# Kernel tuning notes

Hardware: AMD Instinct MI355X
Metric: run time of the kernel (lower is better)

Reference implementation:

```python
import jax, jax.numpy as jnp
import numpy as np
from jax import lax

DN = ('NCDHW', 'OIDHW', 'NCDHW')


def conv3(x, w, stride=1):
    return lax.conv_general_dilated(x, w, (stride,) * 3, 'VALID', dimension_numbers=DN)


def edge_pad(v):  # zero-gradient (Neumann) halo of width 1
    return jnp.pad(v, ((0, 0), (0, 0), (1, 1), (1, 1), (1, 1)), mode='edge')


def zero_pad(v):  # Dirichlet-0 halo for the MG correction
    return jnp.pad(v, ((0, 0), (0, 0), (1, 1), (1, 1), (1, 1)))


def bc_u(u, ub):  # Neumann everywhere, Dirichlet inlet (u=ub) on -x face
    p = edge_pad(u)
    return p.at[:, :, :, :, 0].set(jnp.asarray(ub, p.dtype))


def prol(x):  # nearest-neighbour upsample x2 (nn.Upsample scale_factor=2)
    for ax in (2, 3, 4):
        x = jnp.repeat(x, 2, axis=ax)
    return x


def setup_inputs() -> dict:
    N = 128
    key = jax.random.key(0)
    k = jax.random.split(key, 6)
    shp = (1, 1, N, N, N)
    # 7-point Laplacian stencil (A and diff)
    wA = np.zeros((1, 1, 3, 3, 3), np.float32)
    wA[0, 0, 1, 1, 1] = -6.0
    for d, h, w in [(0, 1, 1), (2, 1, 1), (1, 0, 1), (1, 2, 1), (1, 1, 0), (1, 1, 2)]:
        wA[0, 0, d, h, w] = 1.0
    w_diff = wA.copy()
    # central-difference advection stencils along W (x), H (y), D (z)
    w_xadv = np.zeros((1, 1, 3, 3, 3), np.float32)
    w_xadv[0, 0, 1, 1, 0], w_xadv[0, 0, 1, 1, 2] = -0.5, 0.5
    w_yadv = np.zeros((1, 1, 3, 3, 3), np.float32)
    w_yadv[0, 0, 1, 0, 1], w_yadv[0, 0, 1, 2, 1] = -0.5, 0.5
    w_zadv = np.zeros((1, 1, 3, 3, 3), np.float32)
    w_zadv[0, 0, 0, 1, 1], w_zadv[0, 0, 2, 1, 1] = -0.5, 0.5
    w_res = np.full((1, 1, 2, 2, 2), 0.125, np.float32)
    return {
        'values_u': jax.random.normal(k[0], shp, jnp.float32) * 0.1,
        'values_v': jax.random.normal(k[1], shp, jnp.float32) * 0.1,
        'values_w': jax.random.normal(k[2], shp, jnp.float32) * 0.1,
        'values_p': jax.random.normal(k[3], shp, jnp.float32) * 0.1,
        'sigma': jax.random.uniform(k[4], shp, jnp.float32) * 10.0,  # solid-body drag field
        'dt': jnp.asarray(0.05, jnp.float32),
        'wA': jnp.asarray(wA), 'w_diff': jnp.asarray(w_diff),
        'w_xadv': jnp.asarray(w_xadv), 'w_yadv': jnp.asarray(w_yadv),
        'w_zadv': jnp.asarray(w_zadv), 'w_res': jnp.asarray(w_res),
        'ub': 1, 'Re': 1, 'iteration': 2, 'nlevel': 9,
    }


def reference(values_u, values_v, values_w, values_p, sigma, dt,
              wA, w_diff, w_xadv, w_yadv, w_zadv, w_res,
              ub, Re, iteration, nlevel):
    diag = wA[0, 0, 1, 1, 1]
    A = lambda x: conv3(x, wA)
    diff = lambda x: conv3(x, w_diff)
    xadv = lambda x: conv3(x, w_xadv)
    yadv = lambda x: conv3(x, w_yadv)
    zadv = lambda x: conv3(x, w_zadv)
    res = lambda x: conv3(x, w_res, stride=2)

    def solid(u, v, w):
        f = 1.0 / (1.0 + dt * sigma)
        return u * f, v * f, w * f

    def pg(uu, vv, ww, u, v, w):  # Petrov-Galerkin dissipation (k fields == 1)
        one = jnp.ones_like(u)
        kp = edge_pad(one)
        ku = 0.5 * (one * diff(uu) + diff(uu * kp) - u * diff(kp))
        kv = 0.5 * (one * diff(vv) + diff(vv * kp) - v * diff(kp))
        kw = 0.5 * (one * diff(ww) + diff(ww * kp) - w * diff(kp))
        return ku, kv, kw

    u, v, w = solid(values_u, values_v, values_w)
    uu, vv, ww = bc_u(u, ub), edge_pad(v), edge_pad(w)
    pp = edge_pad(values_p)
    ku, kv, kw = pg(uu, vv, ww, u, v, w)
    # half-step predictor
    b_u = u + 0.5 * (Re * ku * dt - u * xadv(uu) * dt - v * yadv(uu) * dt - w * zadv(uu) * dt) - xadv(pp) * dt
    b_v = v + 0.5 * (Re * kv * dt - u * xadv(vv) * dt - v * yadv(vv) * dt - w * zadv(vv) * dt) - yadv(pp) * dt
    b_w = w + 0.5 * (Re * kw * dt - u * xadv(ww) * dt - v * yadv(ww) * dt - w * zadv(ww) * dt) - zadv(pp) * dt
    b_u, b_v, b_w = solid(b_u, b_v, b_w)
    buu, bvv, bww = bc_u(b_u, ub), edge_pad(b_v), edge_pad(b_w)
    ku, kv, kw = pg(buu, bvv, bww, b_u, b_v, b_w)
    # full-step corrector
    u = u + Re * ku * dt - b_u * xadv(buu) * dt - b_v * yadv(buu) * dt - b_w * zadv(buu) * dt - xadv(pp) * dt
    v = v + Re * kv * dt - b_u * xadv(bvv) * dt - b_v * yadv(bvv) * dt - b_w * zadv(bvv) * dt - yadv(pp) * dt
    w = w + Re * kw * dt - b_u * xadv(bww) * dt - b_v * yadv(bww) * dt - b_w * zadv(bww) * dt - zadv(pp) * dt
    u, v, w = solid(u, v, w)
    uu, vv, ww = bc_u(u, ub), edge_pad(v), edge_pad(w)
    # multigrid F-cycle pressure solve
    b = -(xadv(uu) + yadv(vv) + zadv(ww)) / dt
    p = values_p
    wmg = jnp.zeros((1, 1, 1, 1, 1), u.dtype)
    r = b
    for _ in range(iteration):
        wmg = jnp.zeros((1, 1, 1, 1, 1), u.dtype)
        r = A(pp) - b
        r_s = [r]
        for _i in range(1, nlevel - 1):
            r = res(r)
            r_s.append(r)
        for i in reversed(range(1, nlevel - 1)):
            wp = zero_pad(wmg)
            wmg = wmg - A(wp) / diag + r_s[i] / diag
            wmg = prol(wmg)
        p = p - wmg
        p = p - A(pp) / diag + b / diag
        pp = edge_pad(p)
    u = u - xadv(pp) * dt
    v = v - yadv(pp) * dt
    w = w - zadv(pp) * dt
    u, v, w = solid(u, v, w)
    return u, v, w, p, wmg, r
```

## Files before the change

kernel.cpp:

```cpp
#include <hip/hip_runtime.h>

#define NN 128
#define VV (NN*NN*NN)

typedef float v4 __attribute__((ext_vector_type(4)));
typedef unsigned short u16;

__device__ __forceinline__ float rcpf(float a){ return __builtin_amdgcn_rcpf(a); }
__device__ __forceinline__ v4 rcp4(v4 a){ v4 r; r.x=rcpf(a.x); r.y=rcpf(a.y); r.z=rcpf(a.z); r.w=rcpf(a.w); return r; }
__device__ __forceinline__ v4 mk4(float a,float b,float c,float d){ v4 r; r.x=a;r.y=b;r.z=c;r.w=d; return r; }
__device__ __forceinline__ int clampi(int a, int lo, int hi){ return min(max(a,lo),hi); }

__device__ __forceinline__ float b2f(u16 h){ union{unsigned u; float f;} c; c.u=((unsigned)h)<<16; return c.f; }
__device__ __forceinline__ u16 f2b(float f){
    union{float f; unsigned u;} c; c.f=f;
    unsigned rb = ((c.u>>16)&1u) + 0x7FFFu;
    return (u16)((c.u + rb)>>16);
}
__device__ __forceinline__ float ld1(const float* __restrict__ p, int o){ return p[o]; }
__device__ __forceinline__ float ld1(const u16*  __restrict__ p, int o){ return b2f(p[o]); }
__device__ __forceinline__ v4 ld4(const float* __restrict__ p, int o){ return *(const v4*)(p+o); }
__device__ __forceinline__ v4 ld4(const u16*  __restrict__ p, int o){
    ushort4 h = *(const ushort4*)(p+o);
    return mk4(b2f(h.x),b2f(h.y),b2f(h.z),b2f(h.w));
}
__device__ __forceinline__ void st4(float* __restrict__ p, int o, v4 v){ *(v4*)(p+o) = v; }
__device__ __forceinline__ void st4(u16*  __restrict__ p, int o, v4 v){
    ushort4 h; h.x=f2b(v.x); h.y=f2b(v.y); h.z=f2b(v.z); h.w=f2b(v.w);
    *(ushort4*)(p+o) = h;
}
template<typename T>
__device__ __forceinline__ float ldcT(const T* __restrict__ f, int z, int y, int x){
    z=clampi(z,0,NN-1); y=clampi(y,0,NN-1); x=clampi(x,0,NN-1);
    return ld1(f,(z*NN+y)*NN+x);
}

#define SETUP_OFFS \
    int i4 = (blockIdx.x*blockDim.x + threadIdx.x)<<2; \
    int x = i4 & 127, y = (i4>>7)&127, z = i4>>14; \
    bool x0 = (x==0), x1 = (x==124); \
    int o_c  = i4; \
    int o_ym = o_c + ((y>0)   ? -128   : 0); \
    int o_yp = o_c + ((y<127) ?  128   : 0); \
    int o_zm = o_c + ((z>0)   ? -16384 : 0); \
    int o_zp = o_c + ((z<127) ?  16384 : 0); \
    int o_xm = x0 ? o_c : o_c-1; \
    int o_xp = x1 ? o_c : o_c+4;

__global__ void __launch_bounds__(256) k_predict(
        const float* __restrict__ u_in, const float* __restrict__ v_in,
        const float* __restrict__ w_in, const float* __restrict__ p,
        const float* __restrict__ sg, const float* __restrict__ dtp,
        const int* __restrict__ ubp, const int* __restrict__ rep,
        u16* __restrict__ bu, u16* __restrict__ bv, u16* __restrict__ bw){
    SETUP_OFFS
    float dt = dtp[0], ub = (float)ubp[0], Re = (float)rep[0];
    float h = 0.5f*dt;

    v4 f_c  = rcp4(1.0f + dt*ld4(sg,o_c));
    v4 f_ym = rcp4(1.0f + dt*ld4(sg,o_ym));
    v4 f_yp = rcp4(1.0f + dt*ld4(sg,o_yp));
    v4 f_zm = rcp4(1.0f + dt*ld4(sg,o_zm));
    v4 f_zp = rcp4(1.0f + dt*ld4(sg,o_zp));
    float f_xm = rcpf(1.0f + dt*sg[o_xm]);
    float f_xp = rcpf(1.0f + dt*sg[o_xp]);

#define STEN(F, cen, vxm, vxp, vym, vyp, vzm, vzp, XMVAL) \
    v4 cen = ld4(F,o_c)*f_c; \
    v4 vym = ld4(F,o_ym)*f_ym; v4 vyp = ld4(F,o_yp)*f_yp; \
    v4 vzm = ld4(F,o_zm)*f_zm; v4 vzp = ld4(F,o_zp)*f_zp; \
    float cen##_xms = x0 ? (XMVAL) : F[o_xm]*f_xm; \
    float cen##_xps = x1 ? cen.w   : F[o_xp]*f_xp; \
    v4 vxm = mk4(cen##_xms, cen.x, cen.y, cen.z); \
    v4 vxp = mk4(cen.y, cen.z, cen.w, cen##_xps);

    STEN(u_in, uc, uxm, uxp, uym, uyp, uzm, uzp, ub)
    STEN(v_in, vc, vxm, vxp, vym, vyp, vzm, vzp, vc.x)
    STEN(w_in, wc, wxm, wxp, wym, wyp, wzm, wzp, wc.x)
#undef STEN

    v4 pc = ld4(p,o_c);
    v4 pym = ld4(p,o_ym), pyp = ld4(p,o_yp), pzm = ld4(p,o_zm), pzp = ld4(p,o_zp);
    float p_xms = x0 ? pc.x : p[o_xm];
    float p_xps = x1 ? pc.w : p[o_xp];
    v4 pxm = mk4(p_xms, pc.x, pc.y, pc.z);
    v4 pxp = mk4(pc.y, pc.z, pc.w, p_xps);
    v4 gpx = 0.5f*(pxp-pxm), gpy = 0.5f*(pyp-pym), gpz = 0.5f*(pzp-pzm);

    v4 lap_u = uxm+uxp+uym+uyp+uzm+uzp - 6.0f*uc;
    v4 lap_v = vxm+vxp+vym+vyp+vzm+vzp - 6.0f*vc;
    v4 lap_w = wxm+wxp+wym+wyp+wzm+wzp - 6.0f*wc;
    v4 xau=0.5f*(uxp-uxm), yau=0.5f*(uyp-uym), zau=0.5f*(uzp-uzm);
    v4 xav=0.5f*(vxp-vxm), yav=0.5f*(vyp-vym), zav=0.5f*(vzp-vzm);
    v4 xaw=0.5f*(wxp-wxm), yaw=0.5f*(wyp-wym), zaw=0.5f*(wzp-wzm);

    st4(bu,o_c, (uc + h*(Re*lap_u - (uc*xau + vc*yau + wc*zau)) - dt*gpx)*f_c);
    st4(bv,o_c, (vc + h*(Re*lap_v - (uc*xav + vc*yav + wc*zav)) - dt*gpy)*f_c);
    st4(bw,o_c, (wc + h*(Re*lap_w - (uc*xaw + vc*yaw + wc*zaw)) - dt*gpz)*f_c);
}

__global__ void __launch_bounds__(256) k_corr(
        const float* __restrict__ u_in, const float* __restrict__ v_in,
        const float* __restrict__ w_in,
        const u16* __restrict__ bu, const u16* __restrict__ bv,
        const u16* __restrict__ bw, const float* __restrict__ p,
        const float* __restrict__ sg, const float* __restrict__ dtp,
        const int* __restrict__ ubp, const int* __restrict__ rep,
        u16* __restrict__ ou, u16* __restrict__ ov, u16* __restrict__ ow){
    SETUP_OFFS
    float dt = dtp[0], ub = (float)ubp[0], Re = (float)rep[0];
    v4 f0 = rcp4(1.0f + dt*ld4(sg,o_c));
    v4 u0c = ld4(u_in,o_c)*f0, v0c = ld4(v_in,o_c)*f0, w0c = ld4(w_in,o_c)*f0;

#define STEN2(F, cen, vxm, vxp, vym, vyp, vzm, vzp, XMVAL) \
    v4 cen = ld4(F,o_c); \
    v4 vym = ld4(F,o_ym), vyp = ld4(F,o_yp), vzm = ld4(F,o_zm), vzp = ld4(F,o_zp); \
    float cen##_xms = x0 ? (XMVAL) : ld1(F,o_xm); \
    float cen##_xps = x1 ? cen.w   : ld1(F,o_xp); \
    v4 vxm = mk4(cen##_xms, cen.x, cen.y, cen.z); \
    v4 vxp = mk4(cen.y, cen.z, cen.w, cen##_xps);

    STEN2(bu, uc, uxm, uxp, uym, uyp, uzm, uzp, ub)
    STEN2(bv, vc, vxm, vxp, vym, vyp, vzm, vzp, vc.x)
    STEN2(bw, wc, wxm, wxp, wym, wyp, wzm, wzp, wc.x)
#undef STEN2

    v4 pc = ld4(p,o_c);
    v4 pym = ld4(p,o_ym), pyp = ld4(p,o_yp), pzm = ld4(p,o_zm), pzp = ld4(p,o_zp);
    float p_xms = x0 ? pc.x : p[o_xm];
    float p_xps = x1 ? pc.w : p[o_xp];
    v4 pxm = mk4(p_xms, pc.x, pc.y, pc.z);
    v4 pxp = mk4(pc.y, pc.z, pc.w, p_xps);
    v4 gpx = 0.5f*(pxp-pxm), gpy = 0.5f*(pyp-pym), gpz = 0.5f*(pzp-pzm);

    v4 lap_u = uxm+uxp+uym+uyp+uzm+uzp - 6.0f*uc;
    v4 lap_v = vxm+vxp+vym+vyp+vzm+vzp - 6.0f*vc;
    v4 lap_w = wxm+wxp+wym+wyp+wzm+wzp - 6.0f*wc;
    v4 xau=0.5f*(uxp-uxm), yau=0.5f*(uyp-uym), zau=0.5f*(uzp-uzm);
    v4 xav=0.5f*(vxp-vxm), yav=0.5f*(vyp-vym), zav=0.5f*(vzp-vzm);
    v4 xaw=0.5f*(wxp-wxm), yaw=0.5f*(wyp-wym), zaw=0.5f*(wzp-wzm);

    st4(ou,o_c, (u0c + dt*(Re*lap_u - (uc*xau + vc*yau + wc*zau)) - dt*gpx)*f0);
    st4(ov,o_c, (v0c + dt*(Re*lap_v - (uc*xav + vc*yav + wc*zav)) - dt*gpy)*f0);
    st4(ow,o_c, (w0c + dt*(Re*lap_w - (uc*xaw + vc*yaw + wc*zaw)) - dt*gpz)*f0);
}

__global__ void __launch_bounds__(256) k_div(
        const u16* __restrict__ u, const u16* __restrict__ v,
        const u16* __restrict__ w, const float* __restrict__ dtp,
        const int* __restrict__ ubp, u16* __restrict__ b){
    SETUP_OFFS
    float dt = dtp[0], ub = (float)ubp[0];
    v4 ucv = ld4(u,o_c);
    float u_xms = x0 ? ub    : ld1(u,o_xm);
    float u_xps = x1 ? ucv.w : ld1(u,o_xp);
    v4 uxm = mk4(u_xms, ucv.x, ucv.y, ucv.z);
    v4 uxp = mk4(ucv.y, ucv.z, ucv.w, u_xps);
    v4 vym = ld4(v,o_ym), vyp = ld4(v,o_yp);
    v4 wzm = ld4(w,o_zm), wzp = ld4(w,o_zp);
    v4 div = 0.5f*((uxp-uxm)+(vyp-vym)+(wzp-wzm));
    st4(b,o_c, -div*rcpf(dt));
}

template<typename PT>
__global__ void k_rr(const PT* __restrict__ p, const u16* __restrict__ b, float* __restrict__ r1){
    int i = blockIdx.x*blockDim.x + threadIdx.x;
    if (i >= 64*64*64) return;
    int X = i & 63, Y = (i>>6)&63, Z = i>>12;
    float acc = 0.f;
    #pragma unroll
    for (int dz=0;dz<2;++dz)
      #pragma unroll
      for (int dy=0;dy<2;++dy)
        #pragma unroll
        for (int dx=0;dx<2;++dx){
            int z=2*Z+dz, y=2*Y+dy, x=2*X+dx;
            float pc = ld1(p,(z*128+y)*128+x);
            float lap = ldcT(p,z,y,x-1)+ldcT(p,z,y,x+1)+ldcT(p,z,y-1,x)+ldcT(p,z,y+1,x)
                      + ldcT(p,z-1,y,x)+ldcT(p,z+1,y,x) - 6.0f*pc;
            acc += lap - ld1(b,(z*128+y)*128+x);
        }
    r1[i] = 0.125f*acc;
}

__global__ void k_r2(const float* __restrict__ r1, float* __restrict__ r2){
    int c = blockIdx.x*blockDim.x + threadIdx.x;
    if (c >= 32*32*32) return;
    int X = c & 31, Y = (c>>5)&31, Z = c>>10;
    float a = 0.f;
    #pragma unroll
    for (int dz=0;dz<2;++dz)
      #pragma unroll
      for (int dy=0;dy<2;++dy)
        #pragma unroll
        for (int dx=0;dx<2;++dx)
            a += r1[((2*Z+dz)*64 + (2*Y+dy))*64 + (2*X+dx)];
    r2[c] = 0.125f*a;
}

__device__ void chain_restrict(const float* __restrict__ src, float* __restrict__ dst,
                               int nd, int t, int nt){
    int nd3 = nd*nd*nd, ns = nd*2;
    for (int c = t; c < nd3; c += nt){
        int X = c % nd, Y = (c/nd) % nd, Z = c/(nd*nd);
        float a = 0.f;
        for (int dz=0;dz<2;++dz)
          for (int dy=0;dy<2;++dy)
            for (int dx=0;dx<2;++dx)
                a += src[((2*Z+dz)*ns + (2*Y+dy))*ns + (2*X+dx)];
        dst[c] = 0.125f*a;
    }
}
__device__ void chain_jacobi(const float* __restrict__ jin, const float* __restrict__ r,
                             float* __restrict__ jout, int n, int t, int nt){
    int n3 = n*n*n, hn = n>>1;
    for (int c = t; c < n3; c += nt){
        int X = c % n, Y = (c/n) % n, Z = c/(n*n);
        float s = 0.f;
        s += (X>0  ) ? jin[((Z>>1)*hn+(Y>>1))*hn+((X-1)>>1)] : 0.f;
        s += (X<n-1) ? jin[((Z>>1)*hn+(Y>>1))*hn+((X+1)>>1)] : 0.f;
        s += (Y>0  ) ? jin[((Z>>1)*hn+((Y-1)>>1))*hn+(X>>1)] : 0.f;
        s += (Y<n-1) ? jin[((Z>>1)*hn+((Y+1)>>1))*hn+(X>>1)] : 0.f;
        s += (Z>0  ) ? jin[(((Z-1)>>1)*hn+(Y>>1))*hn+(X>>1)] : 0.f;
        s += (Z<n-1) ? jin[(((Z+1)>>1)*hn+(Y>>1))*hn+(X>>1)] : 0.f;
        jout[c] = (s - r[c]) * (1.0f/6.0f);
    }
}

__global__ void __launch_bounds__(1024) k_chain(const float* __restrict__ r2,
                                                float* __restrict__ j3g, float* __restrict__ r7g){
    __shared__ float r3[4096], r4[512], r5[64], r6[8];
    __shared__ float j7[1], j6[8], j5[64], j4[512], j3[4096];
    int t = threadIdx.x; const int nt = 1024;
    chain_restrict(r2, r3, 16, t, nt); __syncthreads();
    chain_restrict(r3, r4,  8, t, nt); __syncthreads();
    chain_restrict(r4, r5,  4, t, nt); __syncthreads();
    chain_restrict(r5, r6,  2, t, nt); __syncthreads();
    if (t == 0){
        float a = 0.f;
        for (int k=0;k<8;++k) a += r6[k];
        float r7 = 0.125f*a;
        r7g[0] = r7;
        j7[0] = -r7*(1.0f/6.0f);
    }
    __syncthreads();
    chain_jacobi(j7, r6, j6,  2, t, nt); __syncthreads();
    chain_jacobi(j6, r5, j5,  4, t, nt); __syncthreads();
    chain_jacobi(j5, r4, j4,  8, t, nt); __syncthreads();
    chain_jacobi(j4, r3, j3, 16, t, nt); __syncthreads();
    for (int c = t; c < 4096; c += nt) j3g[c] = j3[c];
}

__global__ void k_j2(const float* __restrict__ j3, const float* __restrict__ r2,
                     float* __restrict__ j2){
    int c = blockIdx.x*blockDim.x + threadIdx.x;
    if (c >= 32*32*32) return;
    int X = c & 31, Y = (c>>5)&31, Z = c>>10;
    float s = 0.f;
    s += (X>0 ) ? j3[((Z>>1)*16+(Y>>1))*16+((X-1)>>1)] : 0.f;
    s += (X<31) ? j3[((Z>>1)*16+(Y>>1))*16+((X+1)>>1)] : 0.f;
    s += (Y>0 ) ? j3[((Z>>1)*16+((Y-1)>>1))*16+(X>>1)] : 0.f;
    s += (Y<31) ? j3[((Z>>1)*16+((Y+1)>>1))*16+(X>>1)] : 0.f;
    s += (Z>0 ) ? j3[(((Z-1)>>1)*16+(Y>>1))*16+(X>>1)] : 0.f;
    s += (Z<31) ? j3[(((Z+1)>>1)*16+(Y>>1))*16+(X>>1)] : 0.f;
    j2[c] = (s - r2[c]) * (1.0f/6.0f);
}

__device__ __forceinline__ float j1_eval(const float* __restrict__ r1, const float* __restrict__ j2,
                                         int X, int Y, int Z){
    float s = 0.f;
    s += (X>0 ) ? j2[((Z>>1)*32+(Y>>1))*32+((X-1)>>1)] : 0.f;
    s += (X<63) ? j2[((Z>>1)*32+(Y>>1))*32+((X+1)>>1)] : 0.f;
    s += (Y>0 ) ? j2[((Z>>1)*32+((Y-1)>>1))*32+(X>>1)] : 0.f;
    s += (Y<63) ? j2[((Z>>1)*32+((Y+1)>>1))*32+(X>>1)] : 0.f;
    s += (Z>0 ) ? j2[(((Z-1)>>1)*32+(Y>>1))*32+(X>>1)] : 0.f;
    s += (Z<63) ? j2[(((Z+1)>>1)*32+(Y>>1))*32+(X>>1)] : 0.f;
    return (s - r1[(Z*64+Y)*64+X]) * (1.0f/6.0f);
}

template<typename PT>
__global__ void __launch_bounds__(256) k_pupd(
        const PT* __restrict__ p, const float* __restrict__ r1,
        const float* __restrict__ j2, const u16* __restrict__ b,
        u16* __restrict__ pout){
    SETUP_OFFS
    v4 pc = ld4(p,o_c);
    v4 pym = ld4(p,o_ym), pyp = ld4(p,o_yp), pzm = ld4(p,o_zm), pzp = ld4(p,o_zp);
    float p_xms = x0 ? pc.x : ld1(p,o_xm);
    float p_xps = x1 ? pc.w : ld1(p,o_xp);
    v4 pxm = mk4(p_xms, pc.x, pc.y, pc.z);
    v4 pxp = mk4(pc.y, pc.z, pc.w, p_xps);
    v4 lap = pxm+pxp+pym+pyp+pzm+pzp - 6.0f*pc;
    v4 b4 = ld4(b,o_c);
    float j1a = j1_eval(r1, j2, (x>>1),   y>>1, z>>1);
    float j1b = j1_eval(r1, j2, (x>>1)+1, y>>1, z>>1);
    v4 j1v = mk4(j1a, j1a, j1b, j1b);
    st4(pout,o_c, pc - j1v + (lap - b4)*(1.0f/6.0f));
}

__global__ void __launch_bounds__(256) k_final(
        const u16* __restrict__ u, const u16* __restrict__ v,
        const u16* __restrict__ w, const u16* __restrict__ p,
        const float* __restrict__ r1, const float* __restrict__ j2,
        const float* __restrict__ r7, const float* __restrict__ sg,
        const float* __restrict__ dtp, float* __restrict__ out){
    SETUP_OFFS
    float dt = dtp[0];
    v4 pc = ld4(p,o_c);
    v4 pym = ld4(p,o_ym), pyp = ld4(p,o_yp), pzm = ld4(p,o_zm), pzp = ld4(p,o_zp);
    float p_xms = x0 ? pc.x : ld1(p,o_xm);
    float p_xps = x1 ? pc.w : ld1(p,o_xp);
    v4 pxm = mk4(p_xms, pc.x, pc.y, pc.z);
    v4 pxp = mk4(pc.y, pc.z, pc.w, p_xps);
    v4 gpx = 0.5f*(pxp-pxm), gpy = 0.5f*(pyp-pym), gpz = 0.5f*(pzp-pzm);
    v4 f0 = rcp4(1.0f + dt*ld4(sg,o_c));
    st4(out, o_c,                        (ld4(u,o_c) - dt*gpx)*f0);
    st4(out + (size_t)VV, o_c,           (ld4(v,o_c) - dt*gpy)*f0);
    st4(out + 2*(size_t)VV, o_c,         (ld4(w,o_c) - dt*gpz)*f0);
    st4(out + 3*(size_t)VV, o_c,         pc);
    float j1a = j1_eval(r1, j2, (x>>1),   y>>1, z>>1);
    float j1b = j1_eval(r1, j2, (x>>1)+1, y>>1, z>>1);
    st4(out + 4*(size_t)VV, o_c,         mk4(j1a, j1a, j1b, j1b));
    if (i4 == 0) out[5*(size_t)VV] = r7[0];
}

extern "C" void kernel_launch(void* const* d_in, const int* in_sizes, int n_in,
                              void* d_out, int out_size, void* d_ws, size_t ws_size,
                              hipStream_t stream){
    (void)in_sizes; (void)n_in; (void)out_size; (void)ws_size;
    const float* u_in = (const float*)d_in[0];
    const float* v_in = (const float*)d_in[1];
    const float* w_in = (const float*)d_in[2];
    const float* p_in = (const float*)d_in[3];
    const float* sg   = (const float*)d_in[4];
    const float* dtp  = (const float*)d_in[5];
    const int*  ubp   = (const int*)d_in[12];
    const int*  rep   = (const int*)d_in[13];

    u16* wh = (u16*)d_ws;
    const size_t V = VV;
    u16* bu = wh;
    u16* bv = wh +   V;
    u16* bw = wh + 2*V;
    u16* u  = wh + 3*V;
    u16* v  = wh + 4*V;
    u16* w  = wh + 5*V;
    u16* b  = wh + 6*V;
    u16* P1 = wh + 7*V;
    u16* P2 = wh + 8*V;
    float* fs = (float*)(wh + 10*V);
    float* r1 = fs;
    float* r2 = r1 + 64*64*64;
    float* j2 = r2 + 32*32*32;
    float* j3 = j2 + 32*32*32;
    float* r7 = j3 + 16*16*16;

    dim3 blk(256);
    int g4 = (VV/4)/256;

    k_predict<<<g4, blk, 0, stream>>>(u_in,v_in,w_in,p_in,sg,dtp,ubp,rep,bu,bv,bw);
    k_corr   <<<g4, blk, 0, stream>>>(u_in,v_in,w_in,bu,bv,bw,p_in,sg,dtp,ubp,rep,u,v,w);
    k_div    <<<g4, blk, 0, stream>>>(u,v,w,dtp,ubp,b);

    k_rr<float><<<(64*64*64)/256, blk, 0, stream>>>(p_in, b, r1);
    k_r2        <<<(32*32*32)/256, blk, 0, stream>>>(r1, r2);
    k_chain     <<<1, 1024, 0, stream>>>(r2, j3, r7);
    k_j2        <<<(32*32*32)/256, blk, 0, stream>>>(j3, r2, j2);
    k_pupd<float><<<g4, blk, 0, stream>>>(p_in, r1, j2, b, P1);

    k_rr<u16>  <<<(64*64*64)/256, blk, 0, stream>>>(P1, b, r1);
    k_r2       <<<(32*32*32)/256, blk, 0, stream>>>(r1, r2);
    k_chain    <<<1, 1024, 0, stream>>>(r2, j3, r7);
    k_j2       <<<(32*32*32)/256, blk, 0, stream>>>(j3, r2, j2);
    k_pupd<u16><<<g4, blk, 0, stream>>>(P1, r1, j2, b, P2);

    k_final<<<g4, blk, 0, stream>>>(u,v,w,P2,r1,j2,r7,sg,dtp,(float*)d_out);
}
```

Before: 205.4 us.

## Fuse multigrid stages into tiled kernels with last-block coarse chain

Replaces the chain of divergence, restriction, coarse-chain, prolongation and pressure-update kernels with three tiled kernels on 16^3 blocks. The restrictions run through shared memory, and the last block to finish (found with an atomic counter) runs the coarse-grid chain. The pressure update is recomputed on a halo-padded shared tile and fed straight into the next residual or the final projection, so the P2 buffer and many launches disappear. The costs are redundant halo recomputation, a serial coarse chain inside one block that adds to the tail, and heavy shared-memory use at 512 threads per block, which limits occupancy.

```diff
diff --git a/kernel.cpp b/kernel.cpp
--- a/kernel.cpp
+++ b/kernel.cpp
@@ -2,6 +2,7 @@
 
 #define NN 128
 #define VV (NN*NN*NN)
+#define GRID_MG 512
 
 typedef float v4 __attribute__((ext_vector_type(4)));
 typedef unsigned short u16;
@@ -52,8 +53,10 @@
         const float* __restrict__ w_in, const float* __restrict__ p,
         const float* __restrict__ sg, const float* __restrict__ dtp,
         const int* __restrict__ ubp, const int* __restrict__ rep,
-        u16* __restrict__ bu, u16* __restrict__ bv, u16* __restrict__ bw){
+        u16* __restrict__ bu, u16* __restrict__ bv, u16* __restrict__ bw,
+        int* __restrict__ cnt){
     SETUP_OFFS
+    if (i4 == 0){ cnt[0] = 0; cnt[1] = 0; }
     float dt = dtp[0], ub = (float)ubp[0], Re = (float)rep[0];
     float h = 0.5f*dt;
 
@@ -145,57 +148,16 @@
     st4(ow,o_c, (w0c + dt*(Re*lap_w - (uc*xaw + vc*yaw + wc*zaw)) - dt*gpz)*f0);
 }
 
-__global__ void __launch_bounds__(256) k_div(
-        const u16* __restrict__ u, const u16* __restrict__ v,
-        const u16* __restrict__ w, const float* __restrict__ dtp,
-        const int* __restrict__ ubp, u16* __restrict__ b){
-    SETUP_OFFS
-    float dt = dtp[0], ub = (float)ubp[0];
-    v4 ucv = ld4(u,o_c);
-    float u_xms = x0 ? ub    : ld1(u,o_xm);
-    float u_xps = x1 ? ucv.w : ld1(u,o_xp);
-    v4 uxm = mk4(u_xms, ucv.x, ucv.y, ucv.z);
-    v4 uxp = mk4(ucv.y, ucv.z, ucv.w, u_xps);
-    v4 vym = ld4(v,o_ym), vyp = ld4(v,o_yp);
-    v4 wzm = ld4(w,o_zm), wzp = ld4(w,o_zp);
-    v4 div = 0.5f*((uxp-uxm)+(vyp-vym)+(wzp-wzm));
-    st4(b,o_c, -div*rcpf(dt));
-}
-
-template<typename PT>
-__global__ void k_rr(const PT* __restrict__ p, const u16* __restrict__ b, float* __restrict__ r1){
-    int i = blockIdx.x*blockDim.x + threadIdx.x;
-    if (i >= 64*64*64) return;
-    int X = i & 63, Y = (i>>6)&63, Z = i>>12;
-    float acc = 0.f;
-    #pragma unroll
-    for (int dz=0;dz<2;++dz)
-      #pragma unroll
-      for (int dy=0;dy<2;++dy)
-        #pragma unroll
-        for (int dx=0;dx<2;++dx){
-            int z=2*Z+dz, y=2*Y+dy, x=2*X+dx;
-            float pc = ld1(p,(z*128+y)*128+x);
-            float lap = ldcT(p,z,y,x-1)+ldcT(p,z,y,x+1)+ldcT(p,z,y-1,x)+ldcT(p,z,y+1,x)
-                      + ldcT(p,z-1,y,x)+ldcT(p,z+1,y,x) - 6.0f*pc;
-            acc += lap - ld1(b,(z*128+y)*128+x);
-        }
-    r1[i] = 0.125f*acc;
-}
-
-__global__ void k_r2(const float* __restrict__ r1, float* __restrict__ r2){
-    int c = blockIdx.x*blockDim.x + threadIdx.x;
-    if (c >= 32*32*32) return;
-    int X = c & 31, Y = (c>>5)&31, Z = c>>10;
-    float a = 0.f;
-    #pragma unroll
-    for (int dz=0;dz<2;++dz)
-      #pragma unroll
-      for (int dy=0;dy<2;++dy)
-        #pragma unroll
-        for (int dx=0;dx<2;++dx)
-            a += r1[((2*Z+dz)*64 + (2*Y+dy))*64 + (2*X+dx)];
-    r2[c] = 0.125f*a;
+__device__ __forceinline__ float j1_eval(const float* __restrict__ r1, const float* __restrict__ j2,
+                                         int X, int Y, int Z){
+    float s = 0.f;
+    s += (X>0 ) ? j2[((Z>>1)*32+(Y>>1))*32+((X-1)>>1)] : 0.f;
+    s += (X<63) ? j2[((Z>>1)*32+(Y>>1))*32+((X+1)>>1)] : 0.f;
+    s += (Y>0 ) ? j2[((Z>>1)*32+((Y-1)>>1))*32+(X>>1)] : 0.f;
+    s += (Y<63) ? j2[((Z>>1)*32+((Y+1)>>1))*32+(X>>1)] : 0.f;
+    s += (Z>0 ) ? j2[(((Z-1)>>1)*32+(Y>>1))*32+(X>>1)] : 0.f;
+    s += (Z<63) ? j2[(((Z+1)>>1)*32+(Y>>1))*32+(X>>1)] : 0.f;
+    return (s - r1[(Z*64+Y)*64+X]) * (1.0f/6.0f);
 }
 
 __device__ void chain_restrict(const float* __restrict__ src, float* __restrict__ dst,
@@ -227,101 +189,252 @@
     }
 }
 
-__global__ void __launch_bounds__(1024) k_chain(const float* __restrict__ r2,
-                                                float* __restrict__ j3g, float* __restrict__ r7g){
-    __shared__ float r3[4096], r4[512], r5[64], r6[8];
-    __shared__ float j7[1], j6[8], j5[64], j4[512], j3[4096];
-    int t = threadIdx.x; const int nt = 1024;
-    chain_restrict(r2, r3, 16, t, nt); __syncthreads();
-    chain_restrict(r3, r4,  8, t, nt); __syncthreads();
-    chain_restrict(r4, r5,  4, t, nt); __syncthreads();
-    chain_restrict(r5, r6,  2, t, nt); __syncthreads();
+struct ChainSmem {
+    float r3[4096], r4[512], r5[64], r6[8];
+    float j7[1], j6[8], j5[64], j4[512], j3[4096];
+};
+
+__device__ void run_chain(ChainSmem& S, const float* __restrict__ r2g,
+                          float* __restrict__ j2, float* __restrict__ r7,
+                          int t, int nt){
+    chain_restrict(r2g, S.r3, 16, t, nt); __syncthreads();
+    chain_restrict(S.r3, S.r4,  8, t, nt); __syncthreads();
+    chain_restrict(S.r4, S.r5,  4, t, nt); __syncthreads();
+    chain_restrict(S.r5, S.r6,  2, t, nt); __syncthreads();
     if (t == 0){
         float a = 0.f;
-        for (int k=0;k<8;++k) a += r6[k];
-        float r7 = 0.125f*a;
-        r7g[0] = r7;
-        j7[0] = -r7*(1.0f/6.0f);
-    }
-    __syncthreads();
-    chain_jacobi(j7, r6, j6,  2, t, nt); __syncthreads();
-    chain_jacobi(j6, r5, j5,  4, t, nt); __syncthreads();
-    chain_jacobi(j5, r4, j4,  8, t, nt); __syncthreads();
-    chain_jacobi(j4, r3, j3, 16, t, nt); __syncthreads();
-    for (int c = t; c < 4096; c += nt) j3g[c] = j3[c];
-}
-
-__global__ void k_j2(const float* __restrict__ j3, const float* __restrict__ r2,
-                     float* __restrict__ j2){
-    int c = blockIdx.x*blockDim.x + threadIdx.x;
-    if (c >= 32*32*32) return;
-    int X = c & 31, Y = (c>>5)&31, Z = c>>10;
-    float s = 0.f;
-    s += (X>0 ) ? j3[((Z>>1)*16+(Y>>1))*16+((X-1)>>1)] : 0.f;
-    s += (X<31) ? j3[((Z>>1)*16+(Y>>1))*16+((X+1)>>1)] : 0.f;
-    s += (Y>0 ) ? j3[((Z>>1)*16+((Y-1)>>1))*16+(X>>1)] : 0.f;
-    s += (Y<31) ? j3[((Z>>1)*16+((Y+1)>>1))*16+(X>>1)] : 0.f;
-    s += (Z>0 ) ? j3[(((Z-1)>>1)*16+(Y>>1))*16+(X>>1)] : 0.f;
-    s += (Z<31) ? j3[(((Z+1)>>1)*16+(Y>>1))*16+(X>>1)] : 0.f;
-    j2[c] = (s - r2[c]) * (1.0f/6.0f);
-}
-
-__device__ __forceinline__ float j1_eval(const float* __restrict__ r1, const float* __restrict__ j2,
-                                         int X, int Y, int Z){
-    float s = 0.f;
-    s += (X>0 ) ? j2[((Z>>1)*32+(Y>>1))*32+((X-1)>>1)] : 0.f;
-    s += (X<63) ? j2[((Z>>1)*32+(Y>>1))*32+((X+1)>>1)] : 0.f;
-    s += (Y>0 ) ? j2[((Z>>1)*32+((Y-1)>>1))*32+(X>>1)] : 0.f;
-    s += (Y<63) ? j2[((Z>>1)*32+((Y+1)>>1))*32+(X>>1)] : 0.f;
-    s += (Z>0 ) ? j2[(((Z-1)>>1)*32+(Y>>1))*32+(X>>1)] : 0.f;
-    s += (Z<63) ? j2[(((Z+1)>>1)*32+(Y>>1))*32+(X>>1)] : 0.f;
-    return (s - r1[(Z*64+Y)*64+X]) * (1.0f/6.0f);
+        for (int k=0;k<8;++k) a += S.r6[k];
+        float rv = 0.125f*a;
+        r7[0] = rv;
+        S.j7[0] = -rv*(1.0f/6.0f);
+    }
+    __syncthreads();
+    chain_jacobi(S.j7, S.r6, S.j6,  2, t, nt); __syncthreads();
+    chain_jacobi(S.j6, S.r5, S.j5,  4, t, nt); __syncthreads();
+    chain_jacobi(S.j5, S.r4, S.j4,  8, t, nt); __syncthreads();
+    chain_jacobi(S.j4, S.r3, S.j3, 16, t, nt); __syncthreads();
+    for (int c = t; c < 32*32*32; c += nt){
+        int X = c & 31, Y = (c>>5)&31, Z = c>>10;
+        const float* j3 = S.j3;
+        float s = 0.f;
+        s += (X>0 ) ? j3[((Z>>1)*16+(Y>>1))*16+((X-1)>>1)] : 0.f;
+        s += (X<31) ? j3[((Z>>1)*16+(Y>>1))*16+((X+1)>>1)] : 0.f;
+        s += (Y>0 ) ? j3[((Z>>1)*16+((Y-1)>>1))*16+(X>>1)] : 0.f;
+        s += (Y<31) ? j3[((Z>>1)*16+((Y+1)>>1))*16+(X>>1)] : 0.f;
+        s += (Z>0 ) ? j3[(((Z-1)>>1)*16+(Y>>1))*16+(X>>1)] : 0.f;
+        s += (Z<31) ? j3[(((Z+1)>>1)*16+(Y>>1))*16+(X>>1)] : 0.f;
+        j2[c] = (s - r2g[c]) * (1.0f/6.0f);
+    }
 }
 
 template<typename PT>
-__global__ void __launch_bounds__(256) k_pupd(
-        const PT* __restrict__ p, const float* __restrict__ r1,
-        const float* __restrict__ j2, const u16* __restrict__ b,
-        u16* __restrict__ pout){
-    SETUP_OFFS
-    v4 pc = ld4(p,o_c);
-    v4 pym = ld4(p,o_ym), pyp = ld4(p,o_yp), pzm = ld4(p,o_zm), pzp = ld4(p,o_zp);
-    float p_xms = x0 ? pc.x : ld1(p,o_xm);
-    float p_xps = x1 ? pc.w : ld1(p,o_xp);
-    v4 pxm = mk4(p_xms, pc.x, pc.y, pc.z);
-    v4 pxp = mk4(pc.y, pc.z, pc.w, p_xps);
-    v4 lap = pxm+pxp+pym+pyp+pzm+pzp - 6.0f*pc;
-    v4 b4 = ld4(b,o_c);
-    float j1a = j1_eval(r1, j2, (x>>1),   y>>1, z>>1);
-    float j1b = j1_eval(r1, j2, (x>>1)+1, y>>1, z>>1);
-    v4 j1v = mk4(j1a, j1a, j1b, j1b);
-    st4(pout,o_c, pc - j1v + (lap - b4)*(1.0f/6.0f));
-}
-
-__global__ void __launch_bounds__(256) k_final(
-        const u16* __restrict__ u, const u16* __restrict__ v,
-        const u16* __restrict__ w, const u16* __restrict__ p,
-        const float* __restrict__ r1, const float* __restrict__ j2,
+__device__ void build_P(float* __restrict__ Ps, const PT* __restrict__ p,
+                        const u16* __restrict__ b,
+                        const float* __restrict__ r1x, const float* __restrict__ j2x,
+                        int bx0, int by0, int bz0, int t,
+                        u16* __restrict__ P1out, float* __restrict__ pout){
+    for (int idx = t; idx < 18*18*18; idx += 512){
+        int lx = idx % 18; int tmp = idx/18; int ly = tmp % 18; int lz = tmp/18;
+        int gx = clampi(bx0+lx,0,NN-1), gy = clampi(by0+ly,0,NN-1), gz = clampi(bz0+lz,0,NN-1);
+        int gi = (gz*NN+gy)*NN+gx;
+        float pc = ld1(p, gi);
+        float lap = ldcT(p,gz,gy,gx-1)+ldcT(p,gz,gy,gx+1)+ldcT(p,gz,gy-1,gx)+ldcT(p,gz,gy+1,gx)
+                  + ldcT(p,gz-1,gy,gx)+ldcT(p,gz+1,gy,gx) - 6.0f*pc;
+        float bb = ld1(b, gi);
+        float jv = j1_eval(r1x, j2x, gx>>1, gy>>1, gz>>1);
+        float val = pc - jv + (lap - bb)*(1.0f/6.0f);
+        Ps[idx] = val;
+        if (lx>0 && lx<17 && ly>0 && ly<17 && lz>0 && lz<17){
+            if (P1out) P1out[gi] = f2b(val);
+            if (pout)  pout[gi]  = val;
+        }
+    }
+}
+
+__global__ void __launch_bounds__(512) k_mg1(
+        const u16* __restrict__ u, const u16* __restrict__ v, const u16* __restrict__ w,
+        const float* __restrict__ p, const float* __restrict__ dtp,
+        const int* __restrict__ ubp,
+        u16* __restrict__ b, float* __restrict__ r1, float* __restrict__ r2g,
+        float* __restrict__ j2, float* __restrict__ r7, int* __restrict__ cnt){
+    __shared__ float b_s[16*16*16];
+    __shared__ float r1_s[8*8*8];
+    __shared__ ChainSmem CS;
+    __shared__ int s_last;
+    int t = threadIdx.x;
+    int BX = blockIdx.x & 7, BY = (blockIdx.x>>3)&7, BZ = blockIdx.x>>6;
+    float dt = dtp[0], ub = (float)ubp[0];
+    float rdt = rcpf(dt);
+
+    {
+        int tx4 = t & 3, fy = (t>>2)&15, fz0 = t>>6;
+        int gx = BX*16 + tx4*4, gy = BY*16 + fy;
+        for (int k=0;k<2;++k){
+            int fz = fz0 + 8*k, gz = BZ*16 + fz;
+            int o_c = (gz*NN+gy)*NN + gx;
+            bool x0 = (gx==0), x1 = (gx==124);
+            int o_ym = o_c + ((gy>0)    ? -NN    : 0);
+            int o_yp = o_c + ((gy<NN-1) ?  NN    : 0);
+            int o_zm = o_c + ((gz>0)    ? -NN*NN : 0);
+            int o_zp = o_c + ((gz<NN-1) ?  NN*NN : 0);
+            int o_xm = x0 ? o_c : o_c-1, o_xp = x1 ? o_c : o_c+4;
+            v4 ucv = ld4(u,o_c);
+            float u_xms = x0 ? ub    : ld1(u,o_xm);
+            float u_xps = x1 ? ucv.w : ld1(u,o_xp);
+            v4 uxm = mk4(u_xms, ucv.x, ucv.y, ucv.z);
+            v4 uxp = mk4(ucv.y, ucv.z, ucv.w, u_xps);
+            v4 vym = ld4(v,o_ym), vyp = ld4(v,o_yp);
+            v4 wzm = ld4(w,o_zm), wzp = ld4(w,o_zp);
+            v4 db = -(0.5f*((uxp-uxm)+(vyp-vym)+(wzp-wzm)))*rdt;
+            st4(b,o_c,db);
+            *(v4*)&b_s[(fz*16+fy)*16 + tx4*4] = db;
+        }
+    }
+    __syncthreads();
+    {
+        int CX = t&7, CY = (t>>3)&7, CZ = t>>6;
+        int GX = BX*8+CX, GY = BY*8+CY, GZ = BZ*8+CZ;
+        float acc = 0.f;
+        #pragma unroll
+        for (int dz=0;dz<2;++dz)
+        #pragma unroll
+        for (int dy=0;dy<2;++dy)
+        #pragma unroll
+        for (int dx=0;dx<2;++dx){
+            int z = 2*GZ+dz, y = 2*GY+dy, x = 2*GX+dx;
+            float pc = p[(z*NN+y)*NN+x];
+            float lap = ldcT(p,z,y,x-1)+ldcT(p,z,y,x+1)+ldcT(p,z,y-1,x)+ldcT(p,z,y+1,x)
+                      + ldcT(p,z-1,y,x)+ldcT(p,z+1,y,x) - 6.0f*pc;
+            acc += lap - b_s[((2*CZ+dz)*16+(2*CY+dy))*16+(2*CX+dx)];
+        }
+        float rv = 0.125f*acc;
+        r1[(GZ*64+GY)*64+GX] = rv;
+        r1_s[(CZ*8+CY)*8+CX] = rv;
+    }
+    __syncthreads();
+    if (t < 64){
+        int X = t&3, Y = (t>>2)&3, Z = t>>4;
+        float a = 0.f;
+        #pragma unroll
+        for (int dz=0;dz<2;++dz)
+        #pragma unroll
+        for (int dy=0;dy<2;++dy)
+        #pragma unroll
+        for (int dx=0;dx<2;++dx)
+            a += r1_s[((2*Z+dz)*8+(2*Y+dy))*8+(2*X+dx)];
+        r2g[((BZ*4+Z)*32 + (BY*4+Y))*32 + (BX*4+X)] = 0.125f*a;
+    }
+    __threadfence();
+    __syncthreads();
+    if (t == 0) s_last = (atomicAdd(cnt,1) == GRID_MG-1) ? 1 : 0;
+    __syncthreads();
+    if (!s_last) return;
+    __threadfence();
+    run_chain(CS, r2g, j2, r7, t, 512);
+}
+
+__global__ void __launch_bounds__(512) k_mg2(
+        const float* __restrict__ p, const u16* __restrict__ b,
+        const float* __restrict__ r1a, float* __restrict__ j2,
+        u16* __restrict__ P1, float* __restrict__ r1b,
+        float* __restrict__ r2g, float* __restrict__ r7, int* __restrict__ cnt){
+    __shared__ float Ps[18*18*18];
+    __shared__ float r1_s[8*8*8];
+    __shared__ ChainSmem CS;
+    __shared__ int s_last;
+    int t = threadIdx.x;
+    int BX = blockIdx.x & 7, BY = (blockIdx.x>>3)&7, BZ = blockIdx.x>>6;
+    int bx0 = BX*16-1, by0 = BY*16-1, bz0 = BZ*16-1;
+
+    build_P<float>(Ps, p, b, r1a, j2, bx0,by0,bz0, t, P1, (float*)0);
+    __syncthreads();
+    {
+        int CX = t&7, CY = (t>>3)&7, CZ = t>>6;
+        int GX = BX*8+CX, GY = BY*8+CY, GZ = BZ*8+CZ;
+        float acc = 0.f;
+        #pragma unroll
+        for (int dz=0;dz<2;++dz)
+        #pragma unroll
+        for (int dy=0;dy<2;++dy)
+        #pragma unroll
+        for (int dx=0;dx<2;++dx){
+            int x = 2*GX+dx, y = 2*GY+dy, z = 2*GZ+dz;
+            int lx = x-bx0, ly = y-by0, lz = z-bz0;
+            int lxm = clampi(x-1,0,NN-1)-bx0, lxp = clampi(x+1,0,NN-1)-bx0;
+            int lym = clampi(y-1,0,NN-1)-by0, lyp = clampi(y+1,0,NN-1)-by0;
+            int lzm = clampi(z-1,0,NN-1)-bz0, lzp = clampi(z+1,0,NN-1)-bz0;
+            float pc = Ps[(lz*18+ly)*18+lx];
+            float lap = Ps[(lz*18+ly)*18+lxm] + Ps[(lz*18+ly)*18+lxp]
+                      + Ps[(lz*18+lym)*18+lx] + Ps[(lz*18+lyp)*18+lx]
+                      + Ps[(lzm*18+ly)*18+lx] + Ps[(lzp*18+ly)*18+lx] - 6.0f*pc;
+            acc += lap - ld1(b,(z*NN+y)*NN+x);
+        }
+        float rv = 0.125f*acc;
+        r1b[(GZ*64+GY)*64+GX] = rv;
+        r1_s[(CZ*8+CY)*8+CX] = rv;
+    }
+    __syncthreads();
+    if (t < 64){
+        int X = t&3, Y = (t>>2)&3, Z = t>>4;
+        float a = 0.f;
+        #pragma unroll
+        for (int dz=0;dz<2;++dz)
+        #pragma unroll
+        for (int dy=0;dy<2;++dy)
+        #pragma unroll
+        for (int dx=0;dx<2;++dx)
+            a += r1_s[((2*Z+dz)*8+(2*Y+dy))*8+(2*X+dx)];
+        r2g[((BZ*4+Z)*32 + (BY*4+Y))*32 + (BX*4+X)] = 0.125f*a;
+    }
+    __threadfence();
+    __syncthreads();
+    if (t == 0) s_last = (atomicAdd(cnt,1) == GRID_MG-1) ? 1 : 0;
+    __syncthreads();
+    if (!s_last) return;
+    __threadfence();
+    run_chain(CS, r2g, j2, r7, t, 512);
+}
+
+__global__ void __launch_bounds__(512) k_fin(
+        const u16* __restrict__ u, const u16* __restrict__ v, const u16* __restrict__ w,
+        const u16* __restrict__ P1, const u16* __restrict__ b,
+        const float* __restrict__ r1b, const float* __restrict__ j2,
         const float* __restrict__ r7, const float* __restrict__ sg,
         const float* __restrict__ dtp, float* __restrict__ out){
-    SETUP_OFFS
+    __shared__ float Ps[18*18*18];
+    int t = threadIdx.x;
+    int BX = blockIdx.x & 7, BY = (blockIdx.x>>3)&7, BZ = blockIdx.x>>6;
+    int bx0 = BX*16-1, by0 = BY*16-1, bz0 = BZ*16-1;
+
+    build_P<u16>(Ps, P1, b, r1b, j2, bx0,by0,bz0, t, (u16*)0, out + 3*(size_t)VV);
+    __syncthreads();
+
     float dt = dtp[0];
-    v4 pc = ld4(p,o_c);
-    v4 pym = ld4(p,o_ym), pyp = ld4(p,o_yp), pzm = ld4(p,o_zm), pzp = ld4(p,o_zp);
-    float p_xms = x0 ? pc.x : ld1(p,o_xm);
-    float p_xps = x1 ? pc.w : ld1(p,o_xp);
-    v4 pxm = mk4(p_xms, pc.x, pc.y, pc.z);
-    v4 pxp = mk4(pc.y, pc.z, pc.w, p_xps);
-    v4 gpx = 0.5f*(pxp-pxm), gpy = 0.5f*(pyp-pym), gpz = 0.5f*(pzp-pzm);
-    v4 f0 = rcp4(1.0f + dt*ld4(sg,o_c));
-    st4(out, o_c,                        (ld4(u,o_c) - dt*gpx)*f0);
-    st4(out + (size_t)VV, o_c,           (ld4(v,o_c) - dt*gpy)*f0);
-    st4(out + 2*(size_t)VV, o_c,         (ld4(w,o_c) - dt*gpz)*f0);
-    st4(out + 3*(size_t)VV, o_c,         pc);
-    float j1a = j1_eval(r1, j2, (x>>1),   y>>1, z>>1);
-    float j1b = j1_eval(r1, j2, (x>>1)+1, y>>1, z>>1);
-    st4(out + 4*(size_t)VV, o_c,         mk4(j1a, j1a, j1b, j1b));
-    if (i4 == 0) out[5*(size_t)VV] = r7[0];
+    int tx4 = t & 3, fy = (t>>2)&15, fz0 = t>>6;
+    for (int k=0;k<2;++k){
+        int fz = fz0 + 8*k;
+        int gx = BX*16 + tx4*4, gy = BY*16 + fy, gz = BZ*16 + fz;
+        int o_c = (gz*NN+gy)*NN + gx;
+        int lx = tx4*4+1, ly = fy+1, lz = fz+1;
+        int rb  = (lz*18+ly)*18;
+        float pA = Ps[rb+lx-1], pB = Ps[rb+lx],   pC = Ps[rb+lx+1];
+        float pD = Ps[rb+lx+2], pE = Ps[rb+lx+3], pF = Ps[rb+lx+4];
+        v4 gpx = 0.5f*mk4(pC-pA, pD-pB, pE-pC, pF-pD);
+        int rym = (lz*18+(ly-1))*18, ryp = (lz*18+(ly+1))*18;
+        v4 gpy = 0.5f*mk4(Ps[ryp+lx  ]-Ps[rym+lx  ], Ps[ryp+lx+1]-Ps[rym+lx+1],
+                          Ps[ryp+lx+2]-Ps[rym+lx+2], Ps[ryp+lx+3]-Ps[rym+lx+3]);
+        int rzm = ((lz-1)*18+ly)*18, rzp = ((lz+1)*18+ly)*18;
+        v4 gpz = 0.5f*mk4(Ps[rzp+lx  ]-Ps[rzm+lx  ], Ps[rzp+lx+1]-Ps[rzm+lx+1],
+                          Ps[rzp+lx+2]-Ps[rzm+lx+2], Ps[rzp+lx+3]-Ps[rzm+lx+3]);
+        v4 f0 = rcp4(1.0f + dt*ld4(sg,o_c));
+        st4(out,                o_c, (ld4(u,o_c) - dt*gpx)*f0);
+        st4(out +   (size_t)VV, o_c, (ld4(v,o_c) - dt*gpy)*f0);
+        st4(out + 2*(size_t)VV, o_c, (ld4(w,o_c) - dt*gpz)*f0);
+        float j1a = j1_eval(r1b, j2, (gx>>1),   gy>>1, gz>>1);
+        float j1c = j1_eval(r1b, j2, (gx>>1)+1, gy>>1, gz>>1);
+        st4(out + 4*(size_t)VV, o_c, mk4(j1a, j1a, j1c, j1c));
+    }
+    if (blockIdx.x == 0 && t == 0) out[5*(size_t)VV] = r7[0];
 }
 
 extern "C" void kernel_launch(void* const* d_in, const int* in_sizes, int n_in,
@@ -347,32 +460,20 @@
     u16* w  = wh + 5*V;
     u16* b  = wh + 6*V;
     u16* P1 = wh + 7*V;
-    u16* P2 = wh + 8*V;
-    float* fs = (float*)(wh + 10*V);
-    float* r1 = fs;
-    float* r2 = r1 + 64*64*64;
-    float* j2 = r2 + 32*32*32;
-    float* j3 = j2 + 32*32*32;
-    float* r7 = j3 + 16*16*16;
+    float* fs  = (float*)(wh + 8*V);
+    float* r1a = fs;
+    float* r1b = r1a + 64*64*64;
+    float* r2  = r1b + 64*64*64;
+    float* j2  = r2  + 32*32*32;
+    float* r7  = j2  + 32*32*32;
+    int*   cnt = (int*)(r7 + 1);
 
     dim3 blk(256);
     int g4 = (VV/4)/256;
 
-    k_predict<<<g4, blk, 0, stream>>>(u_in,v_in,w_in,p_in,sg,dtp,ubp,rep,bu,bv,bw);
+    k_predict<<<g4, blk, 0, stream>>>(u_in,v_in,w_in,p_in,sg,dtp,ubp,rep,bu,bv,bw,cnt);
     k_corr   <<<g4, blk, 0, stream>>>(u_in,v_in,w_in,bu,bv,bw,p_in,sg,dtp,ubp,rep,u,v,w);
-    k_div    <<<g4, blk, 0, stream>>>(u,v,w,dtp,ubp,b);
-
-    k_rr<float><<<(64*64*64)/256, blk, 0, stream>>>(p_in, b, r1);
-    k_r2        <<<(32*32*32)/256, blk, 0, stream>>>(r1, r2);
-    k_chain     <<<1, 1024, 0, stream>>>(r2, j3, r7);
-    k_j2        <<<(32*32*32)/256, blk, 0, stream>>>(j3, r2, j2);
-    k_pupd<float><<<g4, blk, 0, stream>>>(p_in, r1, j2, b, P1);
-
-    k_rr<u16>  <<<(64*64*64)/256, blk, 0, stream>>>(P1, b, r1);
-    k_r2       <<<(32*32*32)/256, blk, 0, stream>>>(r1, r2);
-    k_chain    <<<1, 1024, 0, stream>>>(r2, j3, r7);
-    k_j2       <<<(32*32*32)/256, blk, 0, stream>>>(j3, r2, j2);
-    k_pupd<u16><<<g4, blk, 0, stream>>>(P1, r1, j2, b, P2);
-
-    k_final<<<g4, blk, 0, stream>>>(u,v,w,P2,r1,j2,r7,sg,dtp,(float*)d_out);
-}
+    k_mg1<<<GRID_MG, 512, 0, stream>>>(u,v,w,p_in,dtp,ubp,b,r1a,r2,j2,r7,cnt+0);
+    k_mg2<<<GRID_MG, 512, 0, stream>>>(p_in,b,r1a,j2,P1,r1b,r2,r7,cnt+1);
+    k_fin<<<GRID_MG, 512, 0, stream>>>(u,v,w,P1,b,r1b,j2,r7,sg,dtp,(float*)d_out);
+}
```

Result: slower. 450.1 us (+119.2%).
